# Kernel tuning notes

Measured on AMD Instinct MI355X. Metric: run time of the kernel, lower is better.

The kernel has to match this reference:

```python
import jax, jax.numpy as jnp
import numpy as np

EPS = 1e-5


def _conv3x3(x, w):
    # x: [B,C,H,W], w: [O,I,3,3], stride 1, padding 1
    return jax.lax.conv_general_dilated(
        x, w, window_strides=(1, 1), padding=((1, 1), (1, 1)),
        dimension_numbers=("NCHW", "OIHW", "NCHW"))


def _bn(x, g, b, m, v):
    # inference-mode BatchNorm2d over channel dim
    inv = jax.lax.rsqrt(v + EPS) * g
    return x * inv[None, :, None, None] + (b - m * inv)[None, :, None, None]


def setup_inputs() -> dict:
    key = jax.random.key(0)
    B, C, H, W = 32, 256, 56, 56
    ks = jax.random.split(key, 16)
    x = jax.random.normal(ks[0], (B, C, H, W), dtype=jnp.float32)
    mask = (jax.random.uniform(ks[1], (B, 1, H, W)) < 0.5).astype(jnp.float32)
    # dilated mask = 3x3 max-pool of mask
    mask_dilate = jax.lax.reduce_window(
        mask, -jnp.inf, jax.lax.max, (1, 1, 3, 3), (1, 1, 1, 1), "SAME")
    mask_dilate = jnp.maximum(mask_dilate, 0.0).astype(jnp.float32)
    vector = (jax.random.uniform(ks[2], (B, C)) < 0.5).astype(jnp.float32)
    conv1_w = jax.random.normal(ks[3], (C, C, 3, 3), dtype=jnp.float32) * 0.05
    conv2_w = jax.random.normal(ks[4], (C, C, 3, 3), dtype=jnp.float32) * 0.05
    bn1_g = 1.0 + 0.1 * jax.random.normal(ks[5], (C,), dtype=jnp.float32)
    bn1_b = 0.1 * jax.random.normal(ks[6], (C,), dtype=jnp.float32)
    bn1_m = 0.1 * jax.random.normal(ks[7], (C,), dtype=jnp.float32)
    bn1_v = 0.5 + jax.random.uniform(ks[8], (C,), dtype=jnp.float32)
    bn2_g = 1.0 + 0.1 * jax.random.normal(ks[9], (C,), dtype=jnp.float32)
    bn2_b = 0.1 * jax.random.normal(ks[10], (C,), dtype=jnp.float32)
    bn2_m = 0.1 * jax.random.normal(ks[11], (C,), dtype=jnp.float32)
    bn2_v = 0.5 + jax.random.uniform(ks[12], (C,), dtype=jnp.float32)
    return dict(x=x, mask=mask, mask_dilate=mask_dilate, vector=vector,
                conv1_w=conv1_w, bn1_g=bn1_g, bn1_b=bn1_b, bn1_m=bn1_m, bn1_v=bn1_v,
                conv2_w=conv2_w, bn2_g=bn2_g, bn2_b=bn2_b, bn2_m=bn2_m, bn2_v=bn2_v)


def reference(x, mask, mask_dilate, vector,
              conv1_w, bn1_g, bn1_b, bn1_m, bn1_v,
              conv2_w, bn2_g, bn2_b, bn2_m, bn2_v):
    # Sparse BasicBlock, stride=1, no downsample, input_mask=True.
    identity = x
    h = x * mask_dilate                      # apply_mask(x, mask_dilate)
    h = _conv3x3(h, conv1_w) * mask          # conv3x3_mask(conv1, ...)
    h = jax.nn.relu(_bn(h, bn1_g, bn1_b, bn1_m, bn1_v)) * mask_dilate  # bn_relu_mask(bn1, relu, ., mask_dilate)
    h = h * mask                             # apply_mask(x, mask)
    h = h * vector[:, :, None, None]         # channel_process(x, vector)
    h = _conv3x3(h, conv2_w) * mask          # conv3x3_mask(conv2, ...)
    h = _bn(h, bn2_g, bn2_b, bn2_m, bn2_v) * mask  # bn_relu_mask(bn2, None, ., mask)
    out = identity + h * mask                # identity + apply_mask(x, mask)
    return jax.nn.relu(out)
```

## Files before the change

### kernel.cpp

```cpp
#include <hip/hip_runtime.h>
#include <cstdint>


#define EPS 1e-5f

constexpr int Bn = 32, Cc = 256, Hh = 56, Ww = 56;
constexpr int HW = Hh * Ww;
constexpr int WP_ELEMS = 2 * 16 * 9 * 2 * 128 * 8;

typedef __bf16 bf16x8 __attribute__((ext_vector_type(8)));
typedef float  f32x16 __attribute__((ext_vector_type(16)));

__global__ void pack_xm(const float* __restrict__ x, const float* __restrict__ md,
                        __bf16* __restrict__ xm) {
    int blk = blockIdx.x, tid = threadIdx.x;
    int p = tid & 31, cg = tid >> 5;
    int px0 = blk * 32;
    int img = blk / 98;
    int s = (blk - img * 98) * 32 + p;
    float mdv = md[px0 + p];
    #pragma unroll
    for (int it = 0; it < 4; ++it) {
        int c = cg * 8 + it * 64;
        bf16x8 v;
        #pragma unroll
        for (int j = 0; j < 8; ++j)
            v[j] = (__bf16)(x[(size_t)(img * Cc + c + j) * HW + s] * mdv);
        *(bf16x8*)&xm[(size_t)(px0 + p) * Cc + c] = v;
    }
}

__global__ void pack_w(const float* __restrict__ w1, const float* __restrict__ w2,
                       __bf16* __restrict__ wp1, __bf16* __restrict__ wp2) {
    int id = blockIdx.x * 256 + threadIdx.x;
    const float* w = blockIdx.y ? w2 : w1;
    __bf16* wp = blockIdx.y ? wp2 : wp1;
    int j = id & 7; int t = id >> 3;
    int col = t & 127; t >>= 7;
    int half = t & 1; t >>= 1;
    int tap = t % 9; t /= 9;
    int chunk = t & 15; int coblk = t >> 4;
    int co = coblk * 128 + col;
    int ci = chunk * 16 + half * 8 + j;
    wp[id] = (__bf16)(w[((size_t)co * Cc + ci) * 9 + tap]);
}

__global__ void bn_prep(const float* g1, const float* b1, const float* m1, const float* v1,
                        const float* g2, const float* b2, const float* m2, const float* v2,
                        float* binv1, float* bbeta1, float* binv2, float* bbeta2) {
    int c = threadIdx.x;
    float i1 = g1[c] * rsqrtf(v1[c] + EPS);
    binv1[c] = i1; bbeta1[c] = b1[c] - m1[c] * i1;
    float i2 = g2[c] * rsqrtf(v2[c] + EPS);
    binv2[c] = i2; bbeta2[c] = b2[c] - m2[c] * i2;
}

__device__ __forceinline__ void gl_lds16(const __bf16* g, __bf16* l) {
    __builtin_amdgcn_global_load_lds(
        (const __attribute__((address_space(1))) void*)g,
        (__attribute__((address_space(3))) void*)l, 16, 0, 0);
}

template <bool C1>
__global__ __launch_bounds__(256, 2)
void conv_kern(const __bf16* __restrict__ src,
               const __bf16* __restrict__ wp,
               const float* __restrict__ maskg,
               const float* __restrict__ vec,
               const float* __restrict__ binv, const float* __restrict__ bbeta,
               const float* __restrict__ xin,
               void* __restrict__ dstv) {
    __shared__ __align__(16) __bf16 s_in[2 * 6 * 66 * 8];
    __shared__ __align__(16) __bf16 s_w[9 * 2 * 128 * 8];

    const int tid = threadIdx.x;
    const int lane = tid & 63, wave = tid >> 6;
    const int xlane = lane & 31, halfid = lane >> 5;
    const int band = blockIdx.x, coblk = blockIdx.y, img = blockIdx.z;
    const int y0 = band * 4;
    const int co0c = coblk * 128;
    const int pxw = C1 ? (wave >> 1) : (wave & 1);
    const int cow = C1 ? (wave & 1) : (wave >> 1);

    f32x16 acc[4][2];
    #pragma unroll
    for (int a = 0; a < 4; ++a)
        #pragma unroll
        for (int b = 0; b < 2; ++b)
            #pragma unroll
            for (int r = 0; r < 16; ++r) acc[a][b][r] = 0.f;

    const __bf16* wblk = wp + (size_t)coblk * (16 * 9 * 2 * 128 * 8);
    const float* maskp = maskg + (size_t)img * HW;

    for (int chunk = 0; chunk < 16; ++chunk) {
        __syncthreads();
        for (int e = tid; e < 792; e += 256) {
            int half = e & 1, r = e >> 1;
            int yy = r / 66, xx = r - yy * 66;
            int gy = y0 - 1 + yy, gx = xx - 1;
            bf16x8 v = {};
            if ((unsigned)gy < 56u && (unsigned)gx < 56u)
                v = *(const bf16x8*)&src[((size_t)(img * Hh + gy) * Ww + gx) * Cc +
                                          chunk * 16 + half * 8];
            *(bf16x8*)&s_in[((half * 6 + yy) * 66 + xx) * 8] = v;
        }
        {
            const __bf16* g = wblk + (size_t)chunk * (9 * 2 * 128 * 8);
            #pragma unroll
            for (int i = 0; i < 9; ++i) {
                int unit = wave * 576 + i * 64;
                gl_lds16(g + (size_t)(unit + lane) * 8, &s_w[unit * 8]);
            }
        }
        asm volatile("s_waitcnt vmcnt(0)" ::: "memory");
        __syncthreads();

        #pragma unroll
        for (int kh = 0; kh < 3; ++kh)
            #pragma unroll
            for (int kw = 0; kw < 3; ++kw) {
                const int tap = kh * 3 + kw;
                bf16x8 wf[2], inf[4];
                #pragma unroll
                for (int jt = 0; jt < 2; ++jt)
                    wf[jt] = *(const bf16x8*)&s_w[((tap * 2 + halfid) * 128 +
                                                   (cow * 2 + jt) * 32 + xlane) * 8];
                #pragma unroll
                for (int it = 0; it < 4; ++it) {
                    int tg = pxw * 4 + it;
                    int yy = (tg >> 1) + kh;
                    int xx = (tg & 1) * 32 + xlane + kw;
                    inf[it] = *(const bf16x8*)&s_in[((halfid * 6 + yy) * 66 + xx) * 8];
                }
                #pragma unroll
                for (int it = 0; it < 4; ++it)
                    #pragma unroll
                    for (int jt = 0; jt < 2; ++jt) {
                        if constexpr (C1)
                            acc[it][jt] = __builtin_amdgcn_mfma_f32_32x32x16_bf16(
                                inf[it], wf[jt], acc[it][jt], 0, 0, 0);
                        else
                            acc[it][jt] = __builtin_amdgcn_mfma_f32_32x32x16_bf16(
                                wf[jt], inf[it], acc[it][jt], 0, 0, 0);
                    }
            }
    }

    if constexpr (C1) {
        __bf16* u = (__bf16*)dstv;
        float iv[2], bt[2], vv[2]; int cog[2];
        #pragma unroll
        for (int jt = 0; jt < 2; ++jt) {
            cog[jt] = co0c + (cow * 2 + jt) * 32 + xlane;
            iv[jt] = binv[cog[jt]];
            bt[jt] = bbeta[cog[jt]];
            vv[jt] = vec[img * Cc + cog[jt]];
        }
        #pragma unroll
        for (int it = 0; it < 4; ++it) {
            int tg = pxw * 4 + it;
            int y = y0 + (tg >> 1), xb = (tg & 1) * 32;
            #pragma unroll
            for (int reg = 0; reg < 16; ++reg) {
                int x = xb + (reg & 3) + 8 * (reg >> 2) + 4 * halfid;
                if (x < 56) {
                    float mv = maskp[y * 56 + x];
                    size_t base = ((size_t)(img * Hh + y) * Ww + x) * Cc;
                    #pragma unroll
                    for (int jt = 0; jt < 2; ++jt) {
                        float o = fmaxf(fmaf(acc[it][jt][reg], iv[jt], bt[jt]), 0.f)
                                  * mv * vv[jt];
                        u[base + cog[jt]] = (__bf16)o;
                    }
                }
            }
        }
    } else {
        float* outp = (float*)dstv;
        int ya[4], xa[4]; float mva[4]; bool ok[4];
        #pragma unroll
        for (int it = 0; it < 4; ++it) {
            int tg = pxw * 4 + it;
            ya[it] = y0 + (tg >> 1);
            xa[it] = (tg & 1) * 32 + xlane;
            ok[it] = xa[it] < 56;
            mva[it] = ok[it] ? maskp[ya[it] * 56 + xa[it]] : 0.f;
        }
        #pragma unroll
        for (int jt = 0; jt < 2; ++jt) {
            int cb = co0c + (cow * 2 + jt) * 32;
            #pragma unroll
            for (int rg = 0; rg < 4; ++rg) {
                int c4 = cb + 8 * rg + 4 * halfid;
                float4 iv4 = *(const float4*)&binv[c4];
                float4 bt4 = *(const float4*)&bbeta[c4];
                float ivv[4] = {iv4.x, iv4.y, iv4.z, iv4.w};
                float btv[4] = {bt4.x, bt4.y, bt4.z, bt4.w};
                #pragma unroll
                for (int j = 0; j < 4; ++j) {
                    int reg = rg * 4 + j;
                    int co = c4 + j;
                    size_t cbase = (size_t)(img * Cc + co) * HW;
                    #pragma unroll
                    for (int it = 0; it < 4; ++it) {
                        if (ok[it]) {
                            size_t oa = cbase + ya[it] * 56 + xa[it];
                            float o = fmaxf(
                                xin[oa] + mva[it] * fmaf(acc[it][jt][reg], ivv[j], btv[j]),
                                0.f);
                            outp[oa] = o;
                        }
                    }
                }
            }
        }
    }
}

extern "C" void kernel_launch(void* const* d_in, const int* in_sizes, int n_in,
                              void* d_out, int out_size, void* d_ws, size_t ws_size,
                              hipStream_t stream) {
    const float* x    = (const float*)d_in[0];
    const float* mask = (const float*)d_in[1];
    const float* md   = (const float*)d_in[2];
    const float* vec  = (const float*)d_in[3];
    const float* w1   = (const float*)d_in[4];
    const float* bn1g = (const float*)d_in[5];
    const float* bn1b = (const float*)d_in[6];
    const float* bn1m = (const float*)d_in[7];
    const float* bn1v = (const float*)d_in[8];
    const float* w2   = (const float*)d_in[9];
    const float* bn2g = (const float*)d_in[10];
    const float* bn2b = (const float*)d_in[11];
    const float* bn2m = (const float*)d_in[12];
    const float* bn2v = (const float*)d_in[13];
    float* out = (float*)d_out;

    const size_t nhwc = (size_t)Bn * HW * Cc;
    __bf16* xm  = (__bf16*)d_ws;
    __bf16* u   = xm + nhwc;
    __bf16* wp1 = u + nhwc;
    __bf16* wp2 = wp1 + WP_ELEMS;
    float* binv1  = (float*)(wp2 + WP_ELEMS);
    float* bbeta1 = binv1 + 256;
    float* binv2  = bbeta1 + 256;
    float* bbeta2 = binv2 + 256;

    pack_xm<<<dim3(Bn * HW / 32), dim3(256), 0, stream>>>(x, md, xm);
    pack_w<<<dim3(WP_ELEMS / 256, 2), dim3(256), 0, stream>>>(w1, w2, wp1, wp2);
    bn_prep<<<dim3(1), dim3(256), 0, stream>>>(bn1g, bn1b, bn1m, bn1v,
                                               bn2g, bn2b, bn2m, bn2v,
                                               binv1, bbeta1, binv2, bbeta2);

    dim3 grid(14, 2, Bn);
    conv_kern<true><<<grid, dim3(256), 0, stream>>>(
        xm, wp1, mask, vec, binv1, bbeta1, nullptr, u);
    conv_kern<false><<<grid, dim3(256), 0, stream>>>(
        u, wp2, mask, nullptr, binv2, bbeta2, x, out);
}
```

Before: 545.5 us.

## Pad activations spatially, double-buffer LDS with async loads, enlarge conv tiles

Activations are stored in a zero-padded 58x58 NHWC layout so that the conv input tile can be staged straight into LDS with global_load_lds, with no bounds checks. Input and weight tiles are double-buffered so the next channel chunk loads while MFMAs run on the current one, with raised wave priority during compute. Blocks now use 512 threads covering 8 output rows, and a 1D grid is remapped so blocks are spread across XCDs. This adds a halo-zeroing kernel and doubles LDS use, which may limit occupancy.

```diff
diff --git a/kernel.cpp b/kernel.cpp
--- a/kernel.cpp
+++ b/kernel.cpp
@@ -6,6 +6,8 @@
 
 constexpr int Bn = 32, Cc = 256, Hh = 56, Ww = 56;
 constexpr int HW = Hh * Ww;
+constexpr int PD = 58;
+constexpr int PP = PD * PD;
 constexpr int WP_ELEMS = 2 * 16 * 9 * 2 * 128 * 8;
 
 typedef __bf16 bf16x8 __attribute__((ext_vector_type(8)));
@@ -13,20 +15,38 @@
 
 __global__ void pack_xm(const float* __restrict__ x, const float* __restrict__ md,
                         __bf16* __restrict__ xm) {
-    int blk = blockIdx.x, tid = threadIdx.x;
-    int p = tid & 31, cg = tid >> 5;
-    int px0 = blk * 32;
-    int img = blk / 98;
-    int s = (blk - img * 98) * 32 + p;
-    float mdv = md[px0 + p];
-    #pragma unroll
-    for (int it = 0; it < 4; ++it) {
-        int c = cg * 8 + it * 64;
-        bf16x8 v;
-        #pragma unroll
-        for (int j = 0; j < 8; ++j)
-            v[j] = (__bf16)(x[(size_t)(img * Cc + c + j) * HW + s] * mdv);
-        *(bf16x8*)&xm[(size_t)(px0 + p) * Cc + c] = v;
+    int prow = blockIdx.x, img = blockIdx.y;
+    int gy = prow - 1;
+    bool rv = (unsigned)gy < 56u;
+    size_t rowbase = ((size_t)img * PD + prow) * PD * Cc;
+    for (int u = threadIdx.x; u < 32 * 64; u += 256) {
+        int cg = u >> 6, pcol = u & 63;
+        if (pcol >= PD) continue;
+        int gx = pcol - 1;
+        bf16x8 v = {};
+        if (rv && (unsigned)gx < 56u) {
+            float mdv = md[img * HW + gy * 56 + gx];
+            const float* xp = x + ((size_t)img * Cc + cg * 8) * HW + gy * 56 + gx;
+            #pragma unroll
+            for (int j = 0; j < 8; ++j)
+                v[j] = (__bf16)(xp[(size_t)j * HW] * mdv);
+        }
+        *(bf16x8*)&xm[rowbase + (size_t)pcol * Cc + cg * 8] = v;
+    }
+}
+
+__global__ void zero_u_halo(__bf16* __restrict__ u) {
+    int img = blockIdx.x;
+    __bf16* base = u + (size_t)img * PP * Cc;
+    bf16x8 z = {};
+    for (int t = threadIdx.x; t < 228 * 32; t += 256) {
+        int site = t >> 5, cg = (t & 31) * 8;
+        int prow, pcol;
+        if (site < 58)       { prow = 0;          pcol = site; }
+        else if (site < 116) { prow = 57;         pcol = site - 58; }
+        else if (site < 172) { prow = site - 115; pcol = 0; }
+        else                 { prow = site - 171; pcol = 57; }
+        *(bf16x8*)&base[((size_t)prow * PD + pcol) * Cc + cg] = z;
     }
 }
 
@@ -62,7 +82,7 @@
 }
 
 template <bool C1>
-__global__ __launch_bounds__(256, 2)
+__global__ __launch_bounds__(512, 2)
 void conv_kern(const __bf16* __restrict__ src,
                const __bf16* __restrict__ wp,
                const float* __restrict__ maskg,
@@ -70,17 +90,23 @@
                const float* __restrict__ binv, const float* __restrict__ bbeta,
                const float* __restrict__ xin,
                void* __restrict__ dstv) {
-    __shared__ __align__(16) __bf16 s_in[2 * 6 * 66 * 8];
-    __shared__ __align__(16) __bf16 s_w[9 * 2 * 128 * 8];
+    constexpr int SIN1 = 2 * 10 * 66 * 8;
+    constexpr int SW1  = 9 * 2 * 128 * 8;
+    __shared__ __align__(16) __bf16 s_in[2 * SIN1];
+    __shared__ __align__(16) __bf16 s_w[2 * SW1];
 
     const int tid = threadIdx.x;
     const int lane = tid & 63, wave = tid >> 6;
     const int xlane = lane & 31, halfid = lane >> 5;
-    const int band = blockIdx.x, coblk = blockIdx.y, img = blockIdx.z;
-    const int y0 = band * 4;
+    const int pxw = wave >> 1, cow = wave & 1;
+
+    const int bid = blockIdx.x;
+    const int wg = (bid & 7) * 56 + (bid >> 3);
+    const int img = wg / 14;
+    const int t = wg - img * 14;
+    const int y0 = (t >> 1) * 8;
+    const int coblk = t & 1;
     const int co0c = coblk * 128;
-    const int pxw = C1 ? (wave >> 1) : (wave & 1);
-    const int cow = C1 ? (wave & 1) : (wave >> 1);
 
     f32x16 acc[4][2];
     #pragma unroll
@@ -90,32 +116,38 @@
             #pragma unroll
             for (int r = 0; r < 16; ++r) acc[a][b][r] = 0.f;
 
-    const __bf16* wblk = wp + (size_t)coblk * (16 * 9 * 2 * 128 * 8);
+    const __bf16* wblk = wp + (size_t)coblk * (16 * SW1);
     const float* maskp = maskg + (size_t)img * HW;
-
-    for (int chunk = 0; chunk < 16; ++chunk) {
-        __syncthreads();
-        for (int e = tid; e < 792; e += 256) {
-            int half = e & 1, r = e >> 1;
-            int yy = r / 66, xx = r - yy * 66;
-            int gy = y0 - 1 + yy, gx = xx - 1;
-            bf16x8 v = {};
-            if ((unsigned)gy < 56u && (unsigned)gx < 56u)
-                v = *(const bf16x8*)&src[((size_t)(img * Hh + gy) * Ww + gx) * Cc +
-                                          chunk * 16 + half * 8];
-            *(bf16x8*)&s_in[((half * 6 + yy) * 66 + xx) * 8] = v;
-        }
-        {
-            const __bf16* g = wblk + (size_t)chunk * (9 * 2 * 128 * 8);
-            #pragma unroll
-            for (int i = 0; i < 9; ++i) {
-                int unit = wave * 576 + i * 64;
-                gl_lds16(g + (size_t)(unit + lane) * 8, &s_w[unit * 8]);
-            }
-        }
-        asm volatile("s_waitcnt vmcnt(0)" ::: "memory");
-        __syncthreads();
-
+    const __bf16* srcimg = src + (size_t)img * PP * Cc;
+
+    auto STAGE = [&](int b, int chunk) {
+        for (int u0 = wave * 64; u0 < 1320; u0 += 512) {
+            int u = u0 + lane;
+            if (u < 1320) {
+                int half = u / 660, rem = u - half * 660;
+                int row = rem / 66, xx = rem - row * 66;
+                int pcol = xx < PD ? xx : PD - 1;
+                const __bf16* g = srcimg + ((size_t)((y0 + row) * PD + pcol)) * Cc +
+                                  chunk * 16 + half * 8;
+                gl_lds16(g, &s_in[b * SIN1 + u0 * 8]);
+            }
+        }
+        const __bf16* g = wblk + (size_t)chunk * SW1;
+        for (int u0 = wave * 64; u0 < 2304; u0 += 512)
+            gl_lds16(g + (size_t)(u0 + lane) * 8, &s_w[b * SW1 + u0 * 8]);
+    };
+
+    STAGE(0, 0);
+    asm volatile("s_waitcnt vmcnt(0)" ::: "memory");
+    __builtin_amdgcn_s_barrier();
+    __builtin_amdgcn_sched_barrier(0);
+
+    for (int c = 0; c < 16; ++c) {
+        const int b = c & 1;
+        if (c < 15) STAGE(b ^ 1, c + 1);
+        const int sib = b * SIN1, swb = b * SW1;
+
+        __builtin_amdgcn_s_setprio(1);
         #pragma unroll
         for (int kh = 0; kh < 3; ++kh)
             #pragma unroll
@@ -124,14 +156,14 @@
                 bf16x8 wf[2], inf[4];
                 #pragma unroll
                 for (int jt = 0; jt < 2; ++jt)
-                    wf[jt] = *(const bf16x8*)&s_w[((tap * 2 + halfid) * 128 +
+                    wf[jt] = *(const bf16x8*)&s_w[swb + ((tap * 2 + halfid) * 128 +
                                                    (cow * 2 + jt) * 32 + xlane) * 8];
                 #pragma unroll
                 for (int it = 0; it < 4; ++it) {
                     int tg = pxw * 4 + it;
                     int yy = (tg >> 1) + kh;
                     int xx = (tg & 1) * 32 + xlane + kw;
-                    inf[it] = *(const bf16x8*)&s_in[((halfid * 6 + yy) * 66 + xx) * 8];
+                    inf[it] = *(const bf16x8*)&s_in[sib + ((halfid * 10 + yy) * 66 + xx) * 8];
                 }
                 #pragma unroll
                 for (int it = 0; it < 4; ++it)
@@ -145,6 +177,11 @@
                                 wf[jt], inf[it], acc[it][jt], 0, 0, 0);
                     }
             }
+        __builtin_amdgcn_s_setprio(0);
+        __builtin_amdgcn_sched_barrier(0);
+        asm volatile("s_waitcnt vmcnt(0)" ::: "memory");
+        __builtin_amdgcn_s_barrier();
+        __builtin_amdgcn_sched_barrier(0);
     }
 
     if constexpr (C1) {
@@ -166,7 +203,7 @@
                 int x = xb + (reg & 3) + 8 * (reg >> 2) + 4 * halfid;
                 if (x < 56) {
                     float mv = maskp[y * 56 + x];
-                    size_t base = ((size_t)(img * Hh + y) * Ww + x) * Cc;
+                    size_t base = ((size_t)(img * PD + y + 1) * PD + (x + 1)) * Cc;
                     #pragma unroll
                     for (int jt = 0; jt < 2; ++jt) {
                         float o = fmaxf(fmaf(acc[it][jt][reg], iv[jt], bt[jt]), 0.f)
@@ -237,25 +274,25 @@
     const float* bn2v = (const float*)d_in[13];
     float* out = (float*)d_out;
 
-    const size_t nhwc = (size_t)Bn * HW * Cc;
+    const size_t npad = (size_t)Bn * PP * Cc;
     __bf16* xm  = (__bf16*)d_ws;
-    __bf16* u   = xm + nhwc;
-    __bf16* wp1 = u + nhwc;
+    __bf16* u   = xm + npad;
+    __bf16* wp1 = u + npad;
     __bf16* wp2 = wp1 + WP_ELEMS;
     float* binv1  = (float*)(wp2 + WP_ELEMS);
     float* bbeta1 = binv1 + 256;
     float* binv2  = bbeta1 + 256;
     float* bbeta2 = binv2 + 256;
 
-    pack_xm<<<dim3(Bn * HW / 32), dim3(256), 0, stream>>>(x, md, xm);
+    pack_xm<<<dim3(PD, Bn), dim3(256), 0, stream>>>(x, md, xm);
+    zero_u_halo<<<dim3(Bn), dim3(256), 0, stream>>>(u);
     pack_w<<<dim3(WP_ELEMS / 256, 2), dim3(256), 0, stream>>>(w1, w2, wp1, wp2);
     bn_prep<<<dim3(1), dim3(256), 0, stream>>>(bn1g, bn1b, bn1m, bn1v,
                                                bn2g, bn2b, bn2m, bn2v,
                                                binv1, bbeta1, binv2, bbeta2);
 
-    dim3 grid(14, 2, Bn);
-    conv_kern<true><<<grid, dim3(256), 0, stream>>>(
+    conv_kern<true><<<dim3(448), dim3(512), 0, stream>>>(
         xm, wp1, mask, vec, binv1, bbeta1, nullptr, u);
-    conv_kern<false><<<grid, dim3(256), 0, stream>>>(
+    conv_kern<false><<<dim3(448), dim3(512), 0, stream>>>(
         u, wp2, mask, nullptr, binv2, bbeta2, x, out);
 }
```

Result: slower. 593.5 us (+8.8%).
